# Optimization experiments

Hardware: AMD Instinct MI355X
Metric: run time of the kernel (lower is better)

The kernel has to match this reference:

```python
import jax, jax.numpy as jnp
import numpy as np

B, S, D = 8, 4096, 1024
G, V = 2, 320
TAU = 1.0
EPS = 1e-7


def setup_inputs() -> dict:
    key = jax.random.key(0)
    k_x, k_w, k_cb, k_u = jax.random.split(key, 4)
    x = jax.random.normal(k_x, (B, S, D), dtype=jnp.float32)
    W = jax.random.normal(k_w, (D, G * V), dtype=jnp.float32) * (1.0 / np.sqrt(D))
    b = jnp.zeros((G * V,), dtype=jnp.float32)
    # nn.init.uniform_ -> U(0,1); codebooks viewed as [G, V, D//G]
    codebooks = jax.random.uniform(k_cb, (G, V, D // G), dtype=jnp.float32)
    # standard Gumbel(0,1) noise, one per logit: shape [B*S*G, V]
    u = jax.random.uniform(k_u, (B * S * G, V), dtype=jnp.float32,
                           minval=1e-6, maxval=1.0 - 1e-6)
    gumbel = -jnp.log(-jnp.log(u))
    return {"x": x, "W": W, "b": b, "codebooks": codebooks, "gumbel": gumbel}


def reference(x, W, b, codebooks, gumbel):
    Bx, Sx, Dx = x.shape
    Gx, Vx, _ = codebooks.shape
    N = Bx * Sx
    # logit projection: [B,S,D] @ [D, G*V] -> flatten to [N*G, V]
    logits = (jnp.einsum('bsd,de->bse', x, W) + b).reshape(N * Gx, Vx)
    # gumbel-softmax, hard=True with straight-through estimator
    y_soft = jax.nn.softmax((logits + gumbel) / TAU, axis=-1)
    idx = jnp.argmax(y_soft, axis=-1)
    y_hard = jax.nn.one_hot(idx, Vx, dtype=y_soft.dtype)
    one_hot_st = y_hard + y_soft - jax.lax.stop_gradient(y_soft)  # fwd == y_hard
    # codebook lookup via (mostly one-hot) contraction: [N,G,V] x [G,V,d] -> [N,G,d]
    q = jnp.einsum('ngv,gvd->ngd', one_hot_st.reshape(N, Gx, Vx), codebooks)
    quantized = q.reshape(Bx, Sx, Dx)
    # perplexity from clean (non-gumbel) softmax probs
    probs = jax.nn.softmax(logits.reshape(N, Gx, Vx), axis=-1)
    avg_probs = probs.mean(axis=0)  # [G, V]
    perplexity = jnp.exp(-jnp.sum(avg_probs * jnp.log(avg_probs + EPS), axis=-1)).mean()
    return (quantized, perplexity)
```

## Files before the change

kernel.cpp:

```cpp
#include <hip/hip_runtime.h>
#include <hip/hip_bf16.h>
#include <math.h>

#define NROWS 32768
#define DD    1024
#define EE    640
#define VV    320
#define BM    64
#define KT    32
#define CTN   40

typedef __attribute__((ext_vector_type(4))) float float4v;
typedef long long i64t;

static __device__ __forceinline__ void gload_lds16(const void* g, void* l) {
    __builtin_amdgcn_global_load_lds(
        (const __attribute__((address_space(1))) unsigned int*)g,
        (__attribute__((address_space(3))) unsigned int*)l, 16, 0, 0);
}

__global__ void pack_w8(const float* __restrict__ W, unsigned char* __restrict__ bp)
{
    const int t = threadIdx.x;
    const int tile = blockIdx.x * 4 + (t >> 6);
    const int lane = t & 63;
    const int kt = tile / CTN, ct = tile % CTN;
    const int k0 = kt * 32 + (lane >> 4) * 8;
    const int col = ct * 16 + (lane & 15);
    float v[8];
    #pragma unroll
    for (int e = 0; e < 8; ++e)
        v[e] = 16.0f * W[(size_t)(k0 + e) * EE + col];
    int lo = 0, hi = 0;
    lo = __builtin_amdgcn_cvt_pk_fp8_f32(v[0], v[1], lo, false);
    lo = __builtin_amdgcn_cvt_pk_fp8_f32(v[2], v[3], lo, true);
    hi = __builtin_amdgcn_cvt_pk_fp8_f32(v[4], v[5], hi, false);
    hi = __builtin_amdgcn_cvt_pk_fp8_f32(v[6], v[7], hi, true);
    int2 pk; pk.x = lo; pk.y = hi;
    *(int2*)(bp + ((size_t)tile * 64 + lane) * 8) = pk;
}

__global__ __launch_bounds__(512, 4) void fused_vq(
    const float* __restrict__ x, const unsigned char* __restrict__ bp,
    const float* __restrict__ bias, const float* __restrict__ cb,
    const float* __restrict__ gum, float* __restrict__ out,
    float* __restrict__ probs_rep)
{
    __shared__ unsigned char Bs[2][32 * EE];
    __shared__ unsigned char As[2][BM * 32];
    __shared__ float probs_blk[EE];
    __shared__ float pmax[8][BM];
    __shared__ float psum[8][BM];
    __shared__ int   pidx[8][BM];
    __shared__ int   fidx[BM][2];
    __shared__ float finv[BM][2];

    const int t    = threadIdx.x;
    const int lane = t & 63;
    const int cg   = t >> 6;
    const int n0   = blockIdx.x * BM;

    float4v acc[4][5];
    #pragma unroll
    for (int rf = 0; rf < 4; ++rf)
        #pragma unroll
        for (int ct = 0; ct < 5; ++ct)
            acc[rf][ct] = (float4v)0.f;

    const int r0 = t >> 3, kq0 = t & 7;
    const int abase = (r0 >> 4)*512 + ((r0 & 15) + ((kq0 >> 1) << 4))*8 + ((kq0 & 1) << 2);
    const float* xr = x + (size_t)(n0 + r0) * DD + kq0 * 4;

    auto writeA = [&](int bb, float4 v) {
        int pk = 0;
        pk = __builtin_amdgcn_cvt_pk_fp8_f32(v.x, v.y, pk, false);
        pk = __builtin_amdgcn_cvt_pk_fp8_f32(v.z, v.w, pk, true);
        *(int*)&As[bb][abase] = pk;
    };
    auto stageB = [&](int bb, int kt) {
        const unsigned char* src = bp + (size_t)kt * (32 * EE);
        gload_lds16(src + (size_t)t * 16,          &Bs[bb][t * 16]);
        gload_lds16(src + (size_t)(t + 512) * 16,  &Bs[bb][(t + 512) * 16]);
        if (t < 256)
            gload_lds16(src + (size_t)(t + 1024) * 16, &Bs[bb][(t + 1024) * 16]);
    };

    float4 pA = *(const float4*)(xr);
    stageB(0, 0);
    __syncthreads();
    writeA(0, pA);
    __syncthreads();

    for (int kt = 0; kt < KT; ++kt) {
        const int bb = kt & 1;
        const bool more = (kt + 1 < KT);
        if (more) {
            stageB(bb ^ 1, kt + 1);
            pA = *(const float4*)(xr + (kt + 1) * 32);
        }
        i64t af[4];
        #pragma unroll
        for (int rf = 0; rf < 4; ++rf)
            af[rf] = *(const i64t*)&As[bb][rf*512 + lane*8];
        #pragma unroll
        for (int ct = 0; ct < 5; ++ct) {
            i64t bf = *(const i64t*)&Bs[bb][((cg*5 + ct)*64 + lane)*8];
            #pragma unroll
            for (int rf = 0; rf < 4; ++rf)
                acc[rf][ct] = __builtin_amdgcn_mfma_f32_16x16x32_fp8_fp8(af[rf], bf, acc[rf][ct], 0, 0, 0);
        }
        if (more) writeA(bb ^ 1, pA);
        __syncthreads();
    }

    {
        float bv[5];
        #pragma unroll
        for (int ct = 0; ct < 5; ++ct) bv[ct] = bias[cg*80 + ct*16 + (lane & 15)];
        #pragma unroll
        for (int rf = 0; rf < 4; ++rf)
            #pragma unroll
            for (int ct = 0; ct < 5; ++ct)
                #pragma unroll
                for (int r = 0; r < 4; ++r)
                    acc[rf][ct][r] = acc[rf][ct][r] * 0.0625f + bv[ct];
    }

    const int g = cg >> 2;
    const int goff0 = (cg & 3)*80 + (lane & 15);
    #pragma unroll
    for (int rf = 0; rf < 4; ++rf) {
        #pragma unroll
        for (int r = 0; r < 4; ++r) {
            const int rowA = rf*16 + ((lane >> 4) << 2) + r;
            const float* grow = gum + ((size_t)(n0 + rowA)*2 + g)*VV + goff0;
            float m1 = -1e30f; int bi = 0; float es = 0.f;
            #pragma unroll
            for (int ct = 0; ct < 5; ++ct) {
                float zv = acc[rf][ct][r];
                float zg = zv + grow[ct*16];
                if (zg > m1) { m1 = zg; bi = goff0 + ct*16; }
                es += __expf(zv);
            }
            #pragma unroll
            for (int off = 1; off < 16; off <<= 1) {
                float om = __shfl_xor(m1, off);
                int   ob = __shfl_xor(bi, off);
                if (om > m1 || (om == m1 && ob < bi)) { m1 = om; bi = ob; }
                es += __shfl_xor(es, off);
            }
            if ((lane & 15) == 0) {
                pmax[cg][rowA] = m1; pidx[cg][rowA] = bi; psum[cg][rowA] = es;
            }
        }
    }
    for (int c = t; c < EE; c += 512) probs_blk[c] = 0.f;
    __syncthreads();

    if (t < 128) {
        const int row = t & 63, gg = t >> 6;
        float m1 = -1e30f; int bi = 0x7fffffff; float s = 0.f;
        #pragma unroll
        for (int c = 0; c < 4; ++c) {
            const float om = pmax[gg*4 + c][row];
            const int   ob = pidx[gg*4 + c][row];
            if (om > m1 || (om == m1 && ob < bi)) { m1 = om; bi = ob; }
            s += psum[gg*4 + c][row];
        }
        fidx[row][gg] = bi;
        finv[row][gg] = 1.f / s;
    }
    __syncthreads();

    float pacc[5];
    #pragma unroll
    for (int ct = 0; ct < 5; ++ct) pacc[ct] = 0.f;
    #pragma unroll
    for (int rf = 0; rf < 4; ++rf) {
        #pragma unroll
        for (int r = 0; r < 4; ++r) {
            const int rowA = rf*16 + ((lane >> 4) << 2) + r;
            const float inv = finv[rowA][g];
            #pragma unroll
            for (int ct = 0; ct < 5; ++ct)
                pacc[ct] += __expf(acc[rf][ct][r]) * inv;
        }
    }
    #pragma unroll
    for (int off = 16; off < 64; off <<= 1)
        #pragma unroll
        for (int ct = 0; ct < 5; ++ct)
            pacc[ct] += __shfl_xor(pacc[ct], off);
    if (lane < 16) {
        #pragma unroll
        for (int ct = 0; ct < 5; ++ct)
            atomicAdd(&probs_blk[cg*80 + ct*16 + lane], pacc[ct]);
    }
    __syncthreads();

    const int rep = blockIdx.x & 7;
    for (int c = t; c < EE; c += 512)
        atomicAdd(&probs_rep[rep*EE + c], probs_blk[c]);

    for (int i = t; i < BM*256; i += 512) {
        const int row = i >> 8, f4 = i & 255;
        const int gg  = f4 >> 7;
        const int idx = fidx[row][gg];
        const float4 v = *(const float4*)&cb[((size_t)gg*VV + idx)*512 + (size_t)(f4 & 127)*4];
        *(float4*)&out[(size_t)(n0 + row)*DD + (size_t)f4*4] = v;
    }
}

__global__ void perp8_kernel(const float* __restrict__ probs_rep,
                             float* __restrict__ outp)
{
    __shared__ float s0[4], s1[4];
    int t = threadIdx.x;
    float p0 = 0.f, p1 = 0.f;
    for (int c = t; c < EE; c += 256) {
        float a = 0.f;
        #pragma unroll
        for (int rp = 0; rp < 8; ++rp) a += probs_rep[rp*EE + c];
        a *= (1.0f / NROWS);
        float v = a * logf(a + 1e-7f);
        if (c < VV) p0 += v; else p1 += v;
    }
    #pragma unroll
    for (int off = 1; off < 64; off <<= 1) {
        p0 += __shfl_xor(p0, off);
        p1 += __shfl_xor(p1, off);
    }
    if ((t & 63) == 0) { s0[t >> 6] = p0; s1[t >> 6] = p1; }
    __syncthreads();
    if (t == 0) {
        float a0 = s0[0] + s0[1] + s0[2] + s0[3];
        float a1 = s1[0] + s1[1] + s1[2] + s1[3];
        outp[0] = 0.5f * (expf(-a0) + expf(-a1));
    }
}

extern "C" void kernel_launch(void* const* d_in, const int* in_sizes, int n_in,
                              void* d_out, int out_size, void* d_ws, size_t ws_size,
                              hipStream_t stream)
{
    const float* x   = (const float*)d_in[0];
    const float* W   = (const float*)d_in[1];
    const float* b   = (const float*)d_in[2];
    const float* cb  = (const float*)d_in[3];
    const float* gum = (const float*)d_in[4];
    float* out = (float*)d_out;

    char* wsp = (char*)d_ws;
    unsigned char* bp = (unsigned char*)wsp;
    const size_t bp_b = (size_t)DD*EE;
    float* probs_rep = (float*)(wsp + bp_b);
    const size_t pr_b = 8*EE*sizeof(float);

    hipMemsetAsync(probs_rep, 0, pr_b, stream);
    pack_w8<<<320, 256, 0, stream>>>(W, bp);
    fused_vq<<<NROWS / BM, 512, 0, stream>>>(x, bp, b, cb, gum, out, probs_rep);
    perp8_kernel<<<1, 256, 0, stream>>>(probs_rep, out + (out_size - 1));
}
```

Baseline: 116.8 us.

## Retile fused VQ kernel to 128 rows by one group per block

Each block now handles 128 rows and a single codebook group (320 columns) instead of 64 rows and both groups. Each wave covers 64 rows by 80 columns, and the K step doubles to 64. Block indices are remapped so that blocks sharing the same rows and different groups run at different times. The aim is to reuse each staged B tile across more rows and halve the number of K-loop barriers. In exchange, each x row is read and converted to fp8 twice, once per group block, and the grid shrinks to 512 blocks.

Result: slower. 131.8 us (+12.8%).

```diff
diff --git a/kernel.cpp b/kernel.cpp
--- a/kernel.cpp
+++ b/kernel.cpp
@@ -6,8 +6,8 @@
 #define DD    1024
 #define EE    640
 #define VV    320
-#define BM    64
-#define KT    32
+#define BMR   128
+#define KT2   16
 #define CTN   40
 
 typedef __attribute__((ext_vector_type(4))) float float4v;
@@ -46,19 +46,25 @@
     const float* __restrict__ gum, float* __restrict__ out,
     float* __restrict__ probs_rep)
 {
-    __shared__ unsigned char Bs[2][32 * EE];
-    __shared__ unsigned char As[2][BM * 32];
-    __shared__ float probs_blk[EE];
-    __shared__ float pmax[8][BM];
-    __shared__ float psum[8][BM];
-    __shared__ int   pidx[8][BM];
-    __shared__ int   fidx[BM][2];
-    __shared__ float finv[BM][2];
+    __shared__ unsigned char Bs[2][20480];
+    __shared__ unsigned char As[2][8192];
+    __shared__ float probs_blk[VV];
+    __shared__ float pmax[4][BMR];
+    __shared__ float psum[4][BMR];
+    __shared__ int   pidx[4][BMR];
+    __shared__ int   fidx[BMR];
+    __shared__ float finv[BMR];
 
     const int t    = threadIdx.x;
     const int lane = t & 63;
-    const int cg   = t >> 6;
-    const int n0   = blockIdx.x * BM;
+    const int w    = t >> 6;
+    const int rg   = w >> 2;
+    const int cg   = w & 3;
+
+    const int p  = blockIdx.x;
+    const int g  = (p >> 3) & 1;
+    const int rt = (p & 7) * 32 + (p >> 4);
+    const int n0 = rt * BMR;
 
     float4v acc[4][5];
     #pragma unroll
@@ -67,56 +73,77 @@
         for (int ct = 0; ct < 5; ++ct)
             acc[rf][ct] = (float4v)0.f;
 
-    const int r0 = t >> 3, kq0 = t & 7;
-    const int abase = (r0 >> 4)*512 + ((r0 & 15) + ((kq0 >> 1) << 4))*8 + ((kq0 & 1) << 2);
-    const float* xr = x + (size_t)(n0 + r0) * DD + kq0 * 4;
-
-    auto writeA = [&](int bb, float4 v) {
-        int pk = 0;
-        pk = __builtin_amdgcn_cvt_pk_fp8_f32(v.x, v.y, pk, false);
-        pk = __builtin_amdgcn_cvt_pk_fp8_f32(v.z, v.w, pk, true);
-        *(int*)&As[bb][abase] = pk;
+    int aoff[4]; const float* xq[4];
+    #pragma unroll
+    for (int s = 0; s < 4; ++s) {
+        const int Q = t + s * 512;
+        const int row = Q >> 4, kq = Q & 15;
+        aoff[s] = ((row >> 4)*2 + (kq >> 3))*512
+                + ((((kq & 7) >> 1) << 4) + (row & 15))*8 + ((kq & 1) << 2);
+        xq[s] = x + (size_t)(n0 + row) * DD + kq * 4;
+    }
+    auto writeA = [&](int bb, const float4* v) {
+        #pragma unroll
+        for (int s = 0; s < 4; ++s) {
+            int pk = 0;
+            pk = __builtin_amdgcn_cvt_pk_fp8_f32(v[s].x, v[s].y, pk, false);
+            pk = __builtin_amdgcn_cvt_pk_fp8_f32(v[s].z, v[s].w, pk, true);
+            *(int*)&As[bb][aoff[s]] = pk;
+        }
     };
     auto stageB = [&](int bb, int kt) {
-        const unsigned char* src = bp + (size_t)kt * (32 * EE);
-        gload_lds16(src + (size_t)t * 16,          &Bs[bb][t * 16]);
-        gload_lds16(src + (size_t)(t + 512) * 16,  &Bs[bb][(t + 512) * 16]);
-        if (t < 256)
-            gload_lds16(src + (size_t)(t + 1024) * 16, &Bs[bb][(t + 1024) * 16]);
+        const unsigned char* s0 = bp + (((size_t)(2*kt)   * CTN) + g*20) * 512;
+        const unsigned char* s1 = bp + (((size_t)(2*kt+1) * CTN) + g*20) * 512;
+        unsigned char* d = &Bs[bb][0];
+        gload_lds16(s0 + (size_t)t*16, d + t*16);
+        if (t < 128) gload_lds16(s0 + 8192 + (size_t)t*16, d + 8192 + t*16);
+        else         gload_lds16(s1 + (size_t)(t-128)*16,  d + 10240 + (t-128)*16);
+        if (t < 256) gload_lds16(s1 + (size_t)(t+384)*16,  d + 10240 + (t+384)*16);
     };
 
-    float4 pA = *(const float4*)(xr);
+    float4 pA[4];
+    #pragma unroll
+    for (int s = 0; s < 4; ++s) pA[s] = *(const float4*)(xq[s]);
     stageB(0, 0);
     __syncthreads();
     writeA(0, pA);
     __syncthreads();
 
-    for (int kt = 0; kt < KT; ++kt) {
+    for (int kt = 0; kt < KT2; ++kt) {
         const int bb = kt & 1;
-        const bool more = (kt + 1 < KT);
+        const bool more = (kt + 1 < KT2);
+        float4 pN[4];
         if (more) {
             stageB(bb ^ 1, kt + 1);
-            pA = *(const float4*)(xr + (kt + 1) * 32);
-        }
-        i64t af[4];
+            #pragma unroll
+            for (int s = 0; s < 4; ++s)
+                pN[s] = *(const float4*)(xq[s] + (kt + 1) * 64);
+        }
+        i64t af[4][2];
         #pragma unroll
         for (int rf = 0; rf < 4; ++rf)
-            af[rf] = *(const i64t*)&As[bb][rf*512 + lane*8];
-        #pragma unroll
-        for (int ct = 0; ct < 5; ++ct) {
-            i64t bf = *(const i64t*)&Bs[bb][((cg*5 + ct)*64 + lane)*8];
-            #pragma unroll
-            for (int rf = 0; rf < 4; ++rf)
-                acc[rf][ct] = __builtin_amdgcn_mfma_f32_16x16x32_fp8_fp8(af[rf], bf, acc[rf][ct], 0, 0, 0);
-        }
-        if (more) writeA(bb ^ 1, pA);
+            #pragma unroll
+            for (int ks = 0; ks < 2; ++ks)
+                af[rf][ks] = *(const i64t*)&As[bb][((rg*4 + rf)*2 + ks)*512 + lane*8];
+        #pragma unroll
+        for (int ks = 0; ks < 2; ++ks) {
+            #pragma unroll
+            for (int ct = 0; ct < 5; ++ct) {
+                i64t bf = *(const i64t*)&Bs[bb][(ks*20 + cg*5 + ct)*512 + lane*8];
+                #pragma unroll
+                for (int rf = 0; rf < 4; ++rf)
+                    acc[rf][ct] = __builtin_amdgcn_mfma_f32_16x16x32_fp8_fp8(af[rf][ks], bf, acc[rf][ct], 0, 0, 0);
+            }
+        }
+        if (more) writeA(bb ^ 1, pN);
         __syncthreads();
     }
 
+    const int col0 = cg*80 + (lane & 15);
     {
         float bv[5];
         #pragma unroll
-        for (int ct = 0; ct < 5; ++ct) bv[ct] = bias[cg*80 + ct*16 + (lane & 15)];
+        for (int ct = 0; ct < 5; ++ct) bv[ct] = bias[g*VV + col0 + ct*16];
         #pragma unroll
         for (int rf = 0; rf < 4; ++rf)
             #pragma unroll
@@ -126,20 +153,18 @@
                     acc[rf][ct][r] = acc[rf][ct][r] * 0.0625f + bv[ct];
     }
 
-    const int g = cg >> 2;
-    const int goff0 = (cg & 3)*80 + (lane & 15);
     #pragma unroll
     for (int rf = 0; rf < 4; ++rf) {
         #pragma unroll
         for (int r = 0; r < 4; ++r) {
-            const int rowA = rf*16 + ((lane >> 4) << 2) + r;
-            const float* grow = gum + ((size_t)(n0 + rowA)*2 + g)*VV + goff0;
+            const int rowA = rg*64 + rf*16 + ((lane >> 4) << 2) + r;
+            const float* grow = gum + ((size_t)(n0 + rowA)*2 + g)*VV + col0;
             float m1 = -1e30f; int bi = 0; float es = 0.f;
             #pragma unroll
             for (int ct = 0; ct < 5; ++ct) {
                 float zv = acc[rf][ct][r];
                 float zg = zv + grow[ct*16];
-                if (zg > m1) { m1 = zg; bi = goff0 + ct*16; }
+                if (zg > m1) { m1 = zg; bi = col0 + ct*16; }
                 es += __expf(zv);
             }
             #pragma unroll
@@ -154,21 +179,21 @@
             }
         }
     }
-    for (int c = t; c < EE; c += 512) probs_blk[c] = 0.f;
-    __syncthreads();
-
-    if (t < 128) {
-        const int row = t & 63, gg = t >> 6;
+    if (t < VV) probs_blk[t] = 0.f;
+    __syncthreads();
+
+    if (t < BMR) {
+        const int row = t;
         float m1 = -1e30f; int bi = 0x7fffffff; float s = 0.f;
         #pragma unroll
         for (int c = 0; c < 4; ++c) {
-            const float om = pmax[gg*4 + c][row];
-            const int   ob = pidx[gg*4 + c][row];
+            const float om = pmax[c][row];
+            const int   ob = pidx[c][row];
             if (om > m1 || (om == m1 && ob < bi)) { m1 = om; bi = ob; }
-            s += psum[gg*4 + c][row];
-        }
-        fidx[row][gg] = bi;
-        finv[row][gg] = 1.f / s;
+            s += psum[c][row];
+        }
+        fidx[row] = bi;
+        finv[row] = 1.f / s;
     }
     __syncthreads();
 
@@ -179,8 +204,8 @@
     for (int rf = 0; rf < 4; ++rf) {
         #pragma unroll
         for (int r = 0; r < 4; ++r) {
-            const int rowA = rf*16 + ((lane >> 4) << 2) + r;
-            const float inv = finv[rowA][g];
+            const int rowA = rg*64 + rf*16 + ((lane >> 4) << 2) + r;
+            const float inv = finv[rowA];
             #pragma unroll
             for (int ct = 0; ct < 5; ++ct)
                 pacc[ct] += __expf(acc[rf][ct][r]) * inv;
@@ -198,16 +223,15 @@
     }
     __syncthreads();
 
-    const int rep = blockIdx.x & 7;
-    for (int c = t; c < EE; c += 512)
-        atomicAdd(&probs_rep[rep*EE + c], probs_blk[c]);
-
-    for (int i = t; i < BM*256; i += 512) {
-        const int row = i >> 8, f4 = i & 255;
-        const int gg  = f4 >> 7;
-        const int idx = fidx[row][gg];
-        const float4 v = *(const float4*)&cb[((size_t)gg*VV + idx)*512 + (size_t)(f4 & 127)*4];
-        *(float4*)&out[(size_t)(n0 + row)*DD + (size_t)f4*4] = v;
+    const int rep = p & 7;
+    if (t < VV)
+        atomicAdd(&probs_rep[rep*EE + g*VV + t], probs_blk[t]);
+
+    for (int i = t; i < BMR * 128; i += 512) {
+        const int row = i >> 7, f4 = i & 127;
+        const int idx = fidx[row];
+        const float4 v = *(const float4*)&cb[((size_t)g*VV + idx)*512 + (size_t)f4*4];
+        *(float4*)&out[(size_t)(n0 + row)*DD + g*512 + (size_t)f4*4] = v;
     }
 }
 
@@ -258,6 +282,6 @@
 
     hipMemsetAsync(probs_rep, 0, pr_b, stream);
     pack_w8<<<320, 256, 0, stream>>>(W, bp);
-    fused_vq<<<NROWS / BM, 512, 0, stream>>>(x, bp, b, cb, gum, out, probs_rep);
+    fused_vq<<<512, 512, 0, stream>>>(x, bp, b, cb, gum, out, probs_rep);
     perp8_kernel<<<1, 256, 0, stream>>>(probs_rep, out + (out_size - 1));
 }
```

## Triple-buffer B tiles with explicit vmcnt waits and manual unrolled pipeline

Applied to the files above, without the earlier changes.

Moves the B-operand LDS staging from double to triple buffering, prefetching two k-tiles ahead. It manually unrolls the k-loop by two, uses partial s_waitcnt vmcnt plus raw s_barrier and sched_barrier so the next tile's global-to-LDS loads stay in flight across iterations. The aim is to hide global load latency behind the MFMA work. The cost is more LDS per block (possibly lowering occupancy under launch_bounds(512,4)), and it relies on fragile hand-counted wait values. The uniform three loads per thread also re-write some overlapping B chunks.

After: 112.5 us (median of 2 runs). 3.7% less time.

```diff
diff --git a/kernel.cpp b/kernel.cpp
--- a/kernel.cpp
+++ b/kernel.cpp
@@ -46,7 +46,7 @@
     const float* __restrict__ gum, float* __restrict__ out,
     float* __restrict__ probs_rep)
 {
-    __shared__ unsigned char Bs[2][32 * EE];
+    __shared__ unsigned char Bs[3][32 * EE];
     __shared__ unsigned char As[2][BM * 32];
     __shared__ float probs_blk[EE];
     __shared__ float pmax[8][BM];
@@ -79,38 +79,84 @@
     };
     auto stageB = [&](int bb, int kt) {
         const unsigned char* src = bp + (size_t)kt * (32 * EE);
-        gload_lds16(src + (size_t)t * 16,          &Bs[bb][t * 16]);
-        gload_lds16(src + (size_t)(t + 512) * 16,  &Bs[bb][(t + 512) * 16]);
-        if (t < 256)
-            gload_lds16(src + (size_t)(t + 1024) * 16, &Bs[bb][(t + 1024) * 16]);
+        gload_lds16(src + (size_t)t * 16,         &Bs[bb][t * 16]);
+        gload_lds16(src + (size_t)(t + 512) * 16, &Bs[bb][(t + 512) * 16]);
+        const int q2 = (t < 256) ? (t + 1024) : (t + 768);
+        gload_lds16(src + (size_t)q2 * 16, &Bs[bb][q2 * 16]);
     };
-
-    float4 pA = *(const float4*)(xr);
-    stageB(0, 0);
-    __syncthreads();
-    writeA(0, pA);
-    __syncthreads();
-
-    for (int kt = 0; kt < KT; ++kt) {
-        const int bb = kt & 1;
-        const bool more = (kt + 1 < KT);
-        if (more) {
-            stageB(bb ^ 1, kt + 1);
-            pA = *(const float4*)(xr + (kt + 1) * 32);
-        }
-        i64t af[4];
-        #pragma unroll
-        for (int rf = 0; rf < 4; ++rf)
-            af[rf] = *(const i64t*)&As[bb][rf*512 + lane*8];
+    auto mfma5 = [&](int slot, const i64t* af) {
         #pragma unroll
         for (int ct = 0; ct < 5; ++ct) {
-            i64t bf = *(const i64t*)&Bs[bb][((cg*5 + ct)*64 + lane)*8];
+            i64t bf = *(const i64t*)&Bs[slot][((cg*5 + ct)*64 + lane)*8];
             #pragma unroll
             for (int rf = 0; rf < 4; ++rf)
                 acc[rf][ct] = __builtin_amdgcn_mfma_f32_16x16x32_fp8_fp8(af[rf], bf, acc[rf][ct], 0, 0, 0);
         }
-        if (more) writeA(bb ^ 1, pA);
-        __syncthreads();
+    };
+
+    float4 a00 = *(const float4*)(xr);
+    stageB(0, 0);
+    float4 px1 = *(const float4*)(xr + 32);
+    stageB(1, 1);
+    float4 px0;
+    __builtin_amdgcn_sched_barrier(0);
+    writeA(0, a00);
+    asm volatile("s_waitcnt vmcnt(4) lgkmcnt(0)" ::: "memory");
+    __builtin_amdgcn_s_barrier();
+    __builtin_amdgcn_sched_barrier(0);
+
+    int bc = 0;
+    for (int i = 0; i < KT - 2; i += 2) {
+        const int b1 = (bc + 1 > 2) ? 0 : bc + 1;
+        const int b2 = (bc + 2 > 2) ? bc - 1 : bc + 2;
+        {
+            px0 = *(const float4*)(xr + (size_t)(i + 2) * 32);
+            stageB(b2, i + 2);
+            __builtin_amdgcn_sched_barrier(0);
+            i64t af[4];
+            #pragma unroll
+            for (int rf = 0; rf < 4; ++rf)
+                af[rf] = *(const i64t*)&As[0][rf*512 + lane*8];
+            mfma5(bc, af);
+            __builtin_amdgcn_sched_barrier(0);
+            writeA(1, px1);
+            asm volatile("s_waitcnt vmcnt(4) lgkmcnt(0)" ::: "memory");
+            __builtin_amdgcn_s_barrier();
+            __builtin_amdgcn_sched_barrier(0);
+        }
+        {
+            px1 = *(const float4*)(xr + (size_t)(i + 3) * 32);
+            stageB(bc, i + 3);
+            __builtin_amdgcn_sched_barrier(0);
+            i64t af[4];
+            #pragma unroll
+            for (int rf = 0; rf < 4; ++rf)
+                af[rf] = *(const i64t*)&As[1][rf*512 + lane*8];
+            mfma5(b1, af);
+            __builtin_amdgcn_sched_barrier(0);
+            writeA(0, px0);
+            asm volatile("s_waitcnt vmcnt(4) lgkmcnt(0)" ::: "memory");
+            __builtin_amdgcn_s_barrier();
+            __builtin_amdgcn_sched_barrier(0);
+        }
+        bc = b2;
+    }
+    {
+        const int b1 = (bc + 1 > 2) ? 0 : bc + 1;
+        i64t af[4];
+        #pragma unroll
+        for (int rf = 0; rf < 4; ++rf)
+            af[rf] = *(const i64t*)&As[0][rf*512 + lane*8];
+        mfma5(bc, af);
+        __builtin_amdgcn_sched_barrier(0);
+        writeA(1, px1);
+        asm volatile("s_waitcnt vmcnt(0) lgkmcnt(0)" ::: "memory");
+        __builtin_amdgcn_s_barrier();
+        __builtin_amdgcn_sched_barrier(0);
+        #pragma unroll
+        for (int rf = 0; rf < 4; ++rf)
+            af[rf] = *(const i64t*)&As[1][rf*512 + lane*8];
+        mfma5(b1, af);
     }
 
     {
```

## Restructure GEMM main loop with per-wave triple-buffered B and half-K A chunks

Applied to the files above, without the earlier changes.

Replaces the block-wide double-buffered A/B staging with a shared-memory pool. Each wave stages only its own B column slice into a 3-slot ring. Half of the fp8-converted A tile (16 K-steps) is loaded up front, and the second half is prefetched into registers and written at kt==16. Per-iteration __syncthreads are replaced by hand-tuned vmcnt waits and sched_barriers, and epilogue scratch arrays alias the A region to save LDS. The aim is to remove per-step barriers and hide global latency, at the cost of fragile manual waitcnt logic and heavy register use from the prefetched x values.

New measurement: 181.3 us. 1.55x slower.

```diff
diff --git a/kernel.cpp b/kernel.cpp
--- a/kernel.cpp
+++ b/kernel.cpp
@@ -46,14 +46,9 @@
     const float* __restrict__ gum, float* __restrict__ out,
     float* __restrict__ probs_rep)
 {
-    __shared__ unsigned char Bs[2][32 * EE];
-    __shared__ unsigned char As[2][BM * 32];
-    __shared__ float probs_blk[EE];
-    __shared__ float pmax[8][BM];
-    __shared__ float psum[8][BM];
-    __shared__ int   pidx[8][BM];
-    __shared__ int   fidx[BM][2];
-    __shared__ float finv[BM][2];
+    __shared__ __align__(16) unsigned char POOL[77824];
+    unsigned char* Bpool = POOL;
+    unsigned char* Achnk = POOL + 61440;
 
     const int t    = threadIdx.x;
     const int lane = t & 63;
@@ -71,47 +66,103 @@
     const int abase = (r0 >> 4)*512 + ((r0 & 15) + ((kq0 >> 1) << 4))*8 + ((kq0 & 1) << 2);
     const float* xr = x + (size_t)(n0 + r0) * DD + kq0 * 4;
 
-    auto writeA = [&](int bb, float4 v) {
+    unsigned char* Bw = Bpool + cg * 7680;
+    auto stageBp = [&](int slot, int ktS) {
+        const unsigned char* src = bp + ((size_t)ktS * CTN + cg * 5) * 512;
+        unsigned char* d = Bw + slot * 2560;
+        gload_lds16(src + (size_t)lane * 16,        d + lane * 16);
+        gload_lds16(src + (size_t)(64 + lane) * 16, d + (64 + lane) * 16);
+        const int q2 = (lane < 32) ? 128 + lane : 96 + lane;
+        gload_lds16(src + (size_t)q2 * 16, d + q2 * 16);
+    };
+    auto cvtpk = [&](float4 v) {
         int pk = 0;
         pk = __builtin_amdgcn_cvt_pk_fp8_f32(v.x, v.y, pk, false);
         pk = __builtin_amdgcn_cvt_pk_fp8_f32(v.z, v.w, pk, true);
-        *(int*)&As[bb][abase] = pk;
+        return pk;
     };
-    auto stageB = [&](int bb, int kt) {
-        const unsigned char* src = bp + (size_t)kt * (32 * EE);
-        gload_lds16(src + (size_t)t * 16,          &Bs[bb][t * 16]);
-        gload_lds16(src + (size_t)(t + 512) * 16,  &Bs[bb][(t + 512) * 16]);
-        if (t < 256)
-            gload_lds16(src + (size_t)(t + 1024) * 16, &Bs[bb][(t + 1024) * 16]);
-    };
-
-    float4 pA = *(const float4*)(xr);
-    stageB(0, 0);
-    __syncthreads();
-    writeA(0, pA);
-    __syncthreads();
-
+
+    {
+        float4 xa[16];
+        #pragma unroll
+        for (int j = 0; j < 16; ++j)
+            xa[j] = *(const float4*)(xr + j * 32);
+        stageBp(0, 0);
+        stageBp(1, 1);
+        #pragma unroll
+        for (int j = 0; j < 16; ++j)
+            *(int*)&Achnk[j * 2048 + abase] = cvtpk(xa[j]);
+        asm volatile("s_waitcnt vmcnt(3) lgkmcnt(0)" ::: "memory");
+        __builtin_amdgcn_s_barrier();
+        __builtin_amdgcn_sched_barrier(0);
+    }
+
+    float4 xb[16];
+    int    pkv[16];
+
+    #pragma unroll
     for (int kt = 0; kt < KT; ++kt) {
-        const int bb = kt & 1;
-        const bool more = (kt + 1 < KT);
-        if (more) {
-            stageB(bb ^ 1, kt + 1);
-            pA = *(const float4*)(xr + (kt + 1) * 32);
+        if (kt == 16) {
+            __builtin_amdgcn_s_barrier();
+            __builtin_amdgcn_sched_barrier(0);
+            #pragma unroll
+            for (int i = 12; i < 16; ++i) pkv[i] = cvtpk(xb[i]);
+            #pragma unroll
+            for (int j = 0; j < 16; ++j)
+                *(int*)&Achnk[j * 2048 + abase] = pkv[j];
+            asm volatile("s_waitcnt lgkmcnt(0)" ::: "memory");
+            __builtin_amdgcn_s_barrier();
+            __builtin_amdgcn_sched_barrier(0);
+        }
+        {
+            const bool e0 = (kt < 16);
+            const bool b2 = e0 && (kt >= 4) && (((kt - 2) & 3) == 2);
+            const bool b1 = e0 && (kt >= 3) && (((kt - 1) & 3) == 2);
+            const bool k16 = (kt == 16);
+            const int N = (kt == KT - 1) ? 0 : (kt <= 0 ? 7 : (3 + (b2 || k16 ? 4 : 0) + (b1 ? 4 : 0)));
+            if (N == 0)      asm volatile("s_waitcnt vmcnt(0)" ::: "memory");
+            else if (N == 3) asm volatile("s_waitcnt vmcnt(3)" ::: "memory");
+            else             asm volatile("s_waitcnt vmcnt(7)" ::: "memory");
+            __builtin_amdgcn_sched_barrier(0);
         }
         i64t af[4];
         #pragma unroll
         for (int rf = 0; rf < 4; ++rf)
-            af[rf] = *(const i64t*)&As[bb][rf*512 + lane*8];
-        #pragma unroll
-        for (int ct = 0; ct < 5; ++ct) {
-            i64t bf = *(const i64t*)&Bs[bb][((cg*5 + ct)*64 + lane)*8];
+            af[rf] = *(const i64t*)&Achnk[(kt & 15) * 2048 + rf * 512 + lane * 8];
+        i64t bf[5];
+        {
+            const unsigned char* bs = Bw + (kt % 3) * 2560;
+            #pragma unroll
+            for (int ct = 0; ct < 5; ++ct)
+                bf[ct] = *(const i64t*)(bs + ct * 512 + lane * 8);
+        }
+        __builtin_amdgcn_sched_barrier(0);
+        if (kt + 2 < KT) stageBp((kt + 2) % 3, kt + 2);
+        if (kt < 16 && (kt & 3) == 2) {
+            const int b = (kt - 2) >> 2;
+            #pragma unroll
+            for (int i = 0; i < 4; ++i)
+                xb[b * 4 + i] = *(const float4*)(xr + (16 + b * 4 + i) * 32);
+        }
+        if (kt == 6)  { pkv[0] = cvtpk(xb[0]); pkv[1] = cvtpk(xb[1]); pkv[2] = cvtpk(xb[2]); pkv[3] = cvtpk(xb[3]); }
+        if (kt == 10) { pkv[4] = cvtpk(xb[4]); pkv[5] = cvtpk(xb[5]); pkv[6] = cvtpk(xb[6]); pkv[7] = cvtpk(xb[7]); }
+        if (kt == 14) { pkv[8] = cvtpk(xb[8]); pkv[9] = cvtpk(xb[9]); pkv[10] = cvtpk(xb[10]); pkv[11] = cvtpk(xb[11]); }
+        __builtin_amdgcn_sched_barrier(0);
+        #pragma unroll
+        for (int ct = 0; ct < 5; ++ct)
             #pragma unroll
             for (int rf = 0; rf < 4; ++rf)
-                acc[rf][ct] = __builtin_amdgcn_mfma_f32_16x16x32_fp8_fp8(af[rf], bf, acc[rf][ct], 0, 0, 0);
-        }
-        if (more) writeA(bb ^ 1, pA);
-        __syncthreads();
-    }
+                acc[rf][ct] = __builtin_amdgcn_mfma_f32_16x16x32_fp8_fp8(af[rf], bf[ct], acc[rf][ct], 0, 0, 0);
+    }
+
+    __syncthreads();
+
+    float* probs_blk = (float*)(Achnk);
+    float (*pmax)[BM] = (float(*)[BM])(Achnk + 2560);
+    float (*psum)[BM] = (float(*)[BM])(Achnk + 4608);
+    int   (*pidx)[BM] = (int(*)[BM])(Achnk + 6656);
+    int   (*fidx)[2]  = (int(*)[2])(Achnk + 8704);
+    float (*finv)[2]  = (float(*)[2])(Achnk + 9216);
 
     {
         float bv[5];
```
